# Optimization experiments

Measured on AMD Instinct MI355X. Metric: run time of the kernel, lower is better.

## Reference

```python
import jax, jax.numpy as jnp
import numpy as np

D_MODEL = 1024
NHEAD = 16
DK = D_MODEL // NHEAD  # 64
B, S = 2, 2048


def setup_inputs() -> dict:
    key = jax.random.key(0)
    ks = jax.random.split(key, 8)
    Q = jax.random.normal(ks[0], (B, S, D_MODEL), dtype=jnp.float32)
    K = jax.random.normal(ks[1], (B, S, D_MODEL), dtype=jnp.float32)
    V = jax.random.normal(ks[2], (B, S, D_MODEL), dtype=jnp.float32)
    additive_mask = jax.random.normal(ks[3], (S, S), dtype=jnp.float32)
    key_padding_mask = jnp.zeros((B, S), dtype=jnp.int32)  # ignored by the module
    # Per-head projection weights, stacked over heads: [H, d_model, dk]
    scale = 1.0 / np.sqrt(D_MODEL)
    WQ = jax.random.normal(ks[4], (NHEAD, D_MODEL, DK), dtype=jnp.float32) * scale
    WK = jax.random.normal(ks[5], (NHEAD, D_MODEL, DK), dtype=jnp.float32) * scale
    WV = jax.random.normal(ks[6], (NHEAD, D_MODEL, DK), dtype=jnp.float32) * scale
    WO = jax.random.normal(ks[7], (D_MODEL, D_MODEL), dtype=jnp.float32) * scale
    return {"Q": Q, "K": K, "V": V, "additive_mask": additive_mask,
            "key_padding_mask": key_padding_mask,
            "WQ": WQ, "WK": WK, "WV": WV, "WO": WO}


def reference(Q, K, V, additive_mask, key_padding_mask, WQ, WK, WV, WO):
    # Per-head projections, batched over heads: [B, H, S, dk]
    q = jnp.einsum('bsd,hdk->bhsk', Q, WQ)
    k = jnp.einsum('bsd,hdk->bhsk', K, WK)
    v = jnp.einsum('bsd,hdk->bhsk', V, WV)
    # scores: [B, H, S, S]; mask broadcasts over batch and head
    scores = jnp.einsum('bhqk,bhsk->bhqs', q, k) / np.sqrt(DK)
    scores = scores + additive_mask[None, None, :, :]
    attn = jax.nn.softmax(scores, axis=-1)
    o = jnp.einsum('bhqs,bhsk->bhqk', attn, v)  # [B, H, S, dk]
    # concat heads in head order == transpose + reshape to [B, S, H*dk]
    o = o.transpose(0, 2, 1, 3).reshape(Q.shape[0], Q.shape[1], D_MODEL)
    return o @ WO
```

## Files before the change

kernel.cpp:

```cpp
#include <hip/hip_runtime.h>
#include <hip/hip_bf16.h>
#include <stdint.h>

#define D_MODEL 1024
#define NHEAD 16
#define DKH 64
#define BATCH 2
#define SEQ 2048
#define LOG2E 1.44269504088896f

typedef __bf16 bf16_t;
typedef __bf16 bf16x8 __attribute__((ext_vector_type(8)));
typedef float f32x4 __attribute__((ext_vector_type(4)));

__device__ __forceinline__ float fast_exp2(float x) {
#if __has_builtin(__builtin_amdgcn_exp2f)
  return __builtin_amdgcn_exp2f(x);
#else
  return exp2f(x);
#endif
}

__device__ __forceinline__ void gload_lds16(const bf16_t* g, bf16_t* l) {
  auto gp = (const __attribute__((address_space(1))) void*)(uintptr_t)g;
  auto lp = (__attribute__((address_space(3))) void*)(uintptr_t)l;
  __builtin_amdgcn_global_load_lds(gp, lp, 16, 0, 0);
}

__global__ void k_cvt3(const float* __restrict__ Q, const float* __restrict__ K,
                       const float* __restrict__ V, bf16_t* __restrict__ out) {
  const float* in = blockIdx.y == 0 ? Q : (blockIdx.y == 1 ? K : V);
  int i = (blockIdx.x * 256 + threadIdx.x) * 8;
  float4 a = *reinterpret_cast<const float4*>(in + i);
  float4 b = *reinterpret_cast<const float4*>(in + i + 4);
  bf16x8 o;
  o[0] = (bf16_t)a.x; o[1] = (bf16_t)a.y; o[2] = (bf16_t)a.z; o[3] = (bf16_t)a.w;
  o[4] = (bf16_t)b.x; o[5] = (bf16_t)b.y; o[6] = (bf16_t)b.z; o[7] = (bf16_t)b.w;
  *reinterpret_cast<bf16x8*>(out + (size_t)blockIdx.y * BATCH * SEQ * D_MODEL + i) = o;
}

__global__ void k_cvtw(const float* __restrict__ WQ, const float* __restrict__ WK,
                       const float* __restrict__ WV, const float* __restrict__ WO,
                       bf16_t* __restrict__ wt) {
  int j = blockIdx.x * 256 + threadIdx.x;
  int d = j & 1023, n = j >> 10;
  if (n < 3072) {
    int proj = n >> 10, h = (n >> 6) & 15, k = n & 63;
    const float* w = proj == 0 ? WQ : (proj == 1 ? WK : WV);
    float scale = proj == 0 ? (0.125f * LOG2E) : 1.0f;
    wt[j] = (bf16_t)(w[(h << 16) + (d << 6) + k] * scale);
  } else {
    wt[j] = (bf16_t)WO[(d << 10) + (n - 3072)];
  }
}

__global__ void k_maskg(const float* __restrict__ M, bf16_t* __restrict__ Mf) {
  int t = blockIdx.x * 256 + threadIdx.x;
  int c = t & 3, lane = (t >> 2) & 63;
  int kvt = (t >> 8) & 31, qt16 = t >> 13;
  int q = qt16 * 16 + (lane & 15);
  int kv = kvt * 64 + c * 16 + ((lane >> 4) << 2);
  float4 m4 = *reinterpret_cast<const float4*>(M + (size_t)q * SEQ + kv);
  bf16_t o[4];
  o[0] = (bf16_t)(m4.x * LOG2E); o[1] = (bf16_t)(m4.y * LOG2E);
  o[2] = (bf16_t)(m4.z * LOG2E); o[3] = (bf16_t)(m4.w * LOG2E);
  *reinterpret_cast<ushort4*>(Mf + (size_t)t * 4) = *reinterpret_cast<ushort4*>(o);
}

__device__ __forceinline__ int vperm(int u) {
  return ((u >> 5) << 5) | (((u >> 2) & 3) << 3) | (((u >> 4) & 1) << 2) | (u & 3);
}

__global__ __launch_bounds__(256)
void k_gemm_qkv(const bf16_t* __restrict__ A, const bf16_t* __restrict__ Bt,
                bf16_t* __restrict__ qh, bf16_t* __restrict__ kh,
                bf16_t* __restrict__ vT) {
  __shared__ __align__(16) bf16_t As[128 * 32];
  __shared__ __align__(16) bf16_t Bs[128 * 32];
  const int tid = threadIdx.x;
  const int lane = tid & 63, wave = tid >> 6;
  const int g = lane >> 4, lr = lane & 15;
  const int bm = blockIdx.x, bn = blockIdx.y;
  const int pn = bn >> 3;
  const bf16_t* Ap = A + (size_t)pn * (BATCH * SEQ * D_MODEL);
  const int wm = (wave >> 1) << 6, wn = (wave & 1) << 6;
  f32x4 acc[4][4] = {};

  for (int kt = 0; kt < 1024; kt += 32) {
#pragma unroll
    for (int cc = 0; cc < 2; cc++) {
      int c = tid + cc * 256;
      int row = c >> 2, ko = (c & 3) << 3;
      gload_lds16(Ap + (size_t)(bm * 128 + row) * 1024 + kt + ko, As + c * 8);
      gload_lds16(Bt + (size_t)(bn * 128 + row) * 1024 + kt + ko, Bs + c * 8);
    }
    __syncthreads();
    bf16x8 af[4], bfr[4];
#pragma unroll
    for (int t = 0; t < 4; t++)
      af[t] = *reinterpret_cast<const bf16x8*>(As + (wm + t * 16 + lr) * 32 + g * 8);
#pragma unroll
    for (int t = 0; t < 4; t++)
      bfr[t] = *reinterpret_cast<const bf16x8*>(Bs + (wn + t * 16 + lr) * 32 + g * 8);
    __builtin_amdgcn_s_setprio(1);
#pragma unroll
    for (int i = 0; i < 4; i++)
#pragma unroll
      for (int j = 0; j < 4; j++)
        acc[i][j] = __builtin_amdgcn_mfma_f32_16x16x32_bf16(af[i], bfr[j], acc[i][j], 0, 0, 0);
    __builtin_amdgcn_s_setprio(0);
    __syncthreads();
  }

#pragma unroll
  for (int i = 0; i < 4; i++)
#pragma unroll
    for (int j = 0; j < 4; j++)
#pragma unroll
      for (int e = 0; e < 4; e++) {
        int row = (bm << 7) + wm + i * 16 + g * 4 + e;
        int col = ((bn & 7) << 7) + wn + j * 16 + lr;
        float v = acc[i][j][e];
        int b = row >> 11, s = row & 2047, h = col >> 6, kk = col & 63;
        if (pn == 0) {
          qh[((size_t)(((b << 4) + h) * SEQ + s) << 6) + kk] = (bf16_t)v;
        } else if (pn == 1) {
          kh[((size_t)(((b << 4) + h) * SEQ + s) << 6) + kk] = (bf16_t)v;
        } else {
          int s0 = s & ~63, u = s & 63;
          vT[((size_t)((((b << 4) + h) << 6) + kk) << 11) + s0 + vperm(u)] = (bf16_t)v;
        }
      }
}

__global__ __launch_bounds__(256)
void k_gemm_wo(const bf16_t* __restrict__ A, const bf16_t* __restrict__ Bt,
               float* __restrict__ C) {
  __shared__ __align__(16) bf16_t As[64 * 32];
  __shared__ __align__(16) bf16_t Bs[128 * 32];
  const int tid = threadIdx.x;
  const int lane = tid & 63, wave = tid >> 6;
  const int g = lane >> 4, lr = lane & 15;
  const int bm = blockIdx.x, bn = blockIdx.y;
  const int wm = (wave >> 1) << 5, wn = (wave & 1) << 6;
  f32x4 acc[2][4] = {};

  for (int kt = 0; kt < 1024; kt += 32) {
    {
      int row = tid >> 2, ko = (tid & 3) << 3;
      gload_lds16(A + (size_t)(bm * 64 + row) * 1024 + kt + ko, As + tid * 8);
    }
#pragma unroll
    for (int cc = 0; cc < 2; cc++) {
      int c = tid + cc * 256;
      int row = c >> 2, ko = (c & 3) << 3;
      gload_lds16(Bt + (size_t)(bn * 128 + row) * 1024 + kt + ko, Bs + c * 8);
    }
    __syncthreads();
    bf16x8 af[2], bfr[4];
#pragma unroll
    for (int t = 0; t < 2; t++)
      af[t] = *reinterpret_cast<const bf16x8*>(As + (wm + t * 16 + lr) * 32 + g * 8);
#pragma unroll
    for (int t = 0; t < 4; t++)
      bfr[t] = *reinterpret_cast<const bf16x8*>(Bs + (wn + t * 16 + lr) * 32 + g * 8);
    __builtin_amdgcn_s_setprio(1);
#pragma unroll
    for (int i = 0; i < 2; i++)
#pragma unroll
      for (int j = 0; j < 4; j++)
        acc[i][j] = __builtin_amdgcn_mfma_f32_16x16x32_bf16(af[i], bfr[j], acc[i][j], 0, 0, 0);
    __builtin_amdgcn_s_setprio(0);
    __syncthreads();
  }
#pragma unroll
  for (int i = 0; i < 2; i++)
#pragma unroll
    for (int j = 0; j < 4; j++)
#pragma unroll
      for (int e = 0; e < 4; e++) {
        int row = (bm << 6) + wm + i * 16 + g * 4 + e;
        int col = (bn << 7) + wn + j * 16 + lr;
        C[(size_t)row * D_MODEL + col] = acc[i][j][e];
      }
}

__global__ __launch_bounds__(512)
void k_attn4(const bf16_t* __restrict__ Qh, const bf16_t* __restrict__ Kh,
             const bf16_t* __restrict__ VTp, const bf16_t* __restrict__ Mf,
             bf16_t* __restrict__ O) {
  __shared__ __align__(16) bf16_t Ks[2][64 * 64];
  __shared__ __align__(16) bf16_t Vs[2][64 * 64];
  const int bh = blockIdx.y, b = bh >> 4, h = bh & 15;
  const int tid = threadIdx.x, wave = tid >> 6, lane = tid & 63;
  const int g = lane >> 4, lr = lane & 15;
  const int qbase = blockIdx.x * 128 + wave * 16;
  const bf16_t* qp = Qh + (size_t)bh * SEQ * DKH;
  const bf16_t* kp = Kh + (size_t)bh * SEQ * DKH;
  const bf16_t* vp = VTp + (size_t)bh * DKH * SEQ;
  const int qt16 = blockIdx.x * 8 + wave;
  const bf16_t* mp = Mf + ((size_t)qt16 * 32 * 64 + lane) * 16;

  bf16x8 aq[2];
#pragma unroll
  for (int ks = 0; ks < 2; ks++)
    aq[ks] = *reinterpret_cast<const bf16x8*>(
        qp + (size_t)(qbase + lr) * DKH + ks * 32 + g * 8);

  f32x4 oacc[4] = {};
  f32x4 lacc = {};
  const bf16_t onev = (bf16_t)1.0f;
  const bf16x8 ones = {onev, onev, onev, onev, onev, onev, onev, onev};

  auto stage = [&](int buf, int kv0) {
    int r = tid >> 3, u = tid & 7;
    int us = (u ^ (r & 7)) << 3;
    gload_lds16(kp + (size_t)(kv0 + r) * DKH + us, &Ks[buf][tid * 8]);
    gload_lds16(vp + (size_t)r * SEQ + kv0 + us, &Vs[buf][tid * 8]);
  };

  stage(0, 0);
  bf16x8 mva = *reinterpret_cast<const bf16x8*>(mp);
  bf16x8 mvb = *reinterpret_cast<const bf16x8*>(mp + 8);
  __syncthreads();

  for (int it = 0; it < SEQ / 64; ++it) {
    const int cur = it & 1;
    if (it + 1 < SEQ / 64) stage(cur ^ 1, (it + 1) * 64);
    bf16x8 mna = mva, mnb = mvb;
    if (it + 1 < SEQ / 64) {
      const bf16_t* mn = mp + (size_t)(it + 1) * 1024;
      mna = *reinterpret_cast<const bf16x8*>(mn);
      mnb = *reinterpret_cast<const bf16x8*>(mn + 8);
    }

    const bf16_t* kb = Ks[cur];
    const bf16_t* vb = Vs[cur];

    f32x4 p[4];
#pragma unroll
    for (int c = 0; c < 4; c++) {
      int r = c * 16 + lr;
      bf16x8 bk0 = *reinterpret_cast<const bf16x8*>(kb + r * 64 + ((g ^ (lr & 7)) << 3));
      bf16x8 bk1 = *reinterpret_cast<const bf16x8*>(kb + r * 64 + (((4 + g) ^ (lr & 7)) << 3));
      __builtin_amdgcn_s_setprio(1);
      f32x4 a = {};
      a = __builtin_amdgcn_mfma_f32_16x16x32_bf16(bk0, aq[0], a, 0, 0, 0);
      a = __builtin_amdgcn_mfma_f32_16x16x32_bf16(bk1, aq[1], a, 0, 0, 0);
      __builtin_amdgcn_s_setprio(0);
      p[c] = a;
    }

    bf16x8 pa[2];
#pragma unroll
    for (int c = 0; c < 4; c++)
#pragma unroll
      for (int e = 0; e < 4; e++) {
        int idx = c * 4 + e;
        float mk = (float)(idx < 8 ? mva[idx] : mvb[idx - 8]);
        float x = p[c][e] + mk;
        float pe = fast_exp2(fminf(x, 60.f));
        pa[c >> 1][(c & 1) * 4 + e] = (bf16_t)pe;
      }

    lacc = __builtin_amdgcn_mfma_f32_16x16x32_bf16(pa[0], ones, lacc, 0, 0, 0);
    lacc = __builtin_amdgcn_mfma_f32_16x16x32_bf16(pa[1], ones, lacc, 0, 0, 0);

#pragma unroll
    for (int c2 = 0; c2 < 4; c2++) {
      int r = c2 * 16 + lr;
      bf16x8 bv0 = *reinterpret_cast<const bf16x8*>(vb + r * 64 + ((g ^ (lr & 7)) << 3));
      bf16x8 bv1 = *reinterpret_cast<const bf16x8*>(vb + r * 64 + (((4 + g) ^ (lr & 7)) << 3));
      __builtin_amdgcn_s_setprio(1);
      oacc[c2] = __builtin_amdgcn_mfma_f32_16x16x32_bf16(pa[0], bv0, oacc[c2], 0, 0, 0);
      oacc[c2] = __builtin_amdgcn_mfma_f32_16x16x32_bf16(pa[1], bv1, oacc[c2], 0, 0, 0);
      __builtin_amdgcn_s_setprio(0);
    }
    __syncthreads();
    mva = mna; mvb = mnb;
  }

  float inv[4];
#pragma unroll
  for (int e = 0; e < 4; e++) inv[e] = 1.0f / lacc[e];
#pragma unroll
  for (int c2 = 0; c2 < 4; c2++)
#pragma unroll
    for (int e = 0; e < 4; e++) {
      float v = oacc[c2][e] * inv[e];
      int row = qbase + g * 4 + e;
      int col = (h << 6) + c2 * 16 + lr;
      O[(size_t)(b * SEQ + row) * D_MODEL + col] = (bf16_t)v;
    }
}

extern "C" void kernel_launch(void* const* d_in, const int* in_sizes, int n_in,
                              void* d_out, int out_size, void* d_ws, size_t ws_size,
                              hipStream_t stream) {
  const float* Q  = (const float*)d_in[0];
  const float* K  = (const float*)d_in[1];
  const float* V  = (const float*)d_in[2];
  const float* M  = (const float*)d_in[3];
  const float* WQ = (const float*)d_in[5];
  const float* WK = (const float*)d_in[6];
  const float* WV = (const float*)d_in[7];
  const float* WO = (const float*)d_in[8];

  char* ws = (char*)d_ws;
  const size_t MB = 1 << 20;
  bf16_t* Qb    = (bf16_t*)(ws + 0 * MB);
  bf16_t* Mf    = (bf16_t*)(ws + 24 * MB);
  bf16_t* WqkvT = (bf16_t*)(ws + 32 * MB);
  bf16_t* WoT   = (bf16_t*)(ws + 38 * MB);
  bf16_t* qh    = (bf16_t*)(ws + 40 * MB);
  bf16_t* kh    = (bf16_t*)(ws + 48 * MB);
  bf16_t* vT    = (bf16_t*)(ws + 56 * MB);
  bf16_t* Ob    = (bf16_t*)(ws + 64 * MB);

  k_cvt3<<<dim3(2048, 3), 256, 0, stream>>>(Q, K, V, Qb);
  k_maskg<<<4096, 256, 0, stream>>>(M, Mf);
  k_cvtw<<<16384, 256, 0, stream>>>(WQ, WK, WV, WO, WqkvT);

  k_gemm_qkv<<<dim3(32, 24), 256, 0, stream>>>(Qb, WqkvT, qh, kh, vT);

  k_attn4<<<dim3(16, 32), 512, 0, stream>>>(qh, kh, vT, Mf, Ob);

  k_gemm_wo<<<dim3(64, 8), 256, 0, stream>>>(Ob, WoT, (float*)d_out);
}
```

Measured before the change: 152.2 us.

## Rewrite attention with 32x32 MFMA tiles and split-KV across wave halves

Replaces the 16x16x32 MFMA attention kernel with one using 32x32x16 MFMAs. Each group of four waves processes half of the KV sequence, and the two partial outputs and row sums are combined through shared memory at the end. P fragments are repacked with v_permlane32_swap instead of relying on a pre-permuted V layout, so the V transpose write and the mask pre-layout are simplified. The row sum is now a scalar accumulation rather than an MFMA against a ones vector. This aims to cut instruction count and improve MFMA efficiency, at the cost of doubled LDS, a shared-memory reduction step, and a launch bound of 4 blocks per SIMD that may pressure registers.

```diff
diff --git a/kernel.cpp b/kernel.cpp
--- a/kernel.cpp
+++ b/kernel.cpp
@@ -12,6 +12,7 @@
 typedef __bf16 bf16_t;
 typedef __bf16 bf16x8 __attribute__((ext_vector_type(8)));
 typedef float f32x4 __attribute__((ext_vector_type(4)));
+typedef float f32x16 __attribute__((ext_vector_type(16)));
 
 __device__ __forceinline__ float fast_exp2(float x) {
 #if __has_builtin(__builtin_amdgcn_exp2f)
@@ -25,6 +26,18 @@
   auto gp = (const __attribute__((address_space(1))) void*)(uintptr_t)g;
   auto lp = (__attribute__((address_space(3))) void*)(uintptr_t)l;
   __builtin_amdgcn_global_load_lds(gp, lp, 16, 0, 0);
+}
+
+__device__ __forceinline__ uint32_t pkbf(float lo, float hi) {
+  bf16_t a = (bf16_t)lo, c = (bf16_t)hi;
+  uint16_t ua, uc;
+  __builtin_memcpy(&ua, &a, 2);
+  __builtin_memcpy(&uc, &c, 2);
+  return (uint32_t)ua | ((uint32_t)uc << 16);
+}
+
+__device__ __forceinline__ void perm32swap(uint32_t& a, uint32_t& b) {
+  asm volatile("v_permlane32_swap_b32 %0, %1" : "+v"(a), "+v"(b));
 }
 
 __global__ void k_cvt3(const float* __restrict__ Q, const float* __restrict__ K,
@@ -56,19 +69,17 @@
 
 __global__ void k_maskg(const float* __restrict__ M, bf16_t* __restrict__ Mf) {
   int t = blockIdx.x * 256 + threadIdx.x;
-  int c = t & 3, lane = (t >> 2) & 63;
-  int kvt = (t >> 8) & 31, qt16 = t >> 13;
-  int q = qt16 * 16 + (lane & 15);
-  int kv = kvt * 64 + c * 16 + ((lane >> 4) << 2);
-  float4 m4 = *reinterpret_cast<const float4*>(M + (size_t)q * SEQ + kv);
+  int wch = t & 7, lane = (t >> 3) & 63;
+  int kvt = (t >> 9) & 31, qt = t >> 14;
+  int h = lane >> 5, ql = lane & 31;
+  int q = qt * 32 + ql;
+  int t32 = wch >> 2, r2 = wch & 3;
+  int kvb = kvt * 64 + t32 * 32 + 8 * r2 + 4 * h;
+  float4 m4 = *reinterpret_cast<const float4*>(M + (size_t)q * SEQ + kvb);
   bf16_t o[4];
   o[0] = (bf16_t)(m4.x * LOG2E); o[1] = (bf16_t)(m4.y * LOG2E);
   o[2] = (bf16_t)(m4.z * LOG2E); o[3] = (bf16_t)(m4.w * LOG2E);
   *reinterpret_cast<ushort4*>(Mf + (size_t)t * 4) = *reinterpret_cast<ushort4*>(o);
-}
-
-__device__ __forceinline__ int vperm(int u) {
-  return ((u >> 5) << 5) | (((u >> 2) & 3) << 3) | (((u >> 4) & 1) << 2) | (u & 3);
 }
 
 __global__ __launch_bounds__(256)
@@ -127,8 +138,7 @@
         } else if (pn == 1) {
           kh[((size_t)(((b << 4) + h) * SEQ + s) << 6) + kk] = (bf16_t)v;
         } else {
-          int s0 = s & ~63, u = s & 63;
-          vT[((size_t)((((b << 4) + h) << 6) + kk) << 11) + s0 + vperm(u)] = (bf16_t)v;
+          vT[((size_t)((((b << 4) + h) << 6) + kk) << 11) + s] = (bf16_t)v;
         }
       }
 }
@@ -185,113 +195,163 @@
       }
 }
 
-__global__ __launch_bounds__(512)
-void k_attn4(const bf16_t* __restrict__ Qh, const bf16_t* __restrict__ Kh,
-             const bf16_t* __restrict__ VTp, const bf16_t* __restrict__ Mf,
+__global__ __launch_bounds__(512, 4)
+void k_attn5(const bf16_t* __restrict__ Qh, const bf16_t* __restrict__ Kh,
+             const bf16_t* __restrict__ VT, const bf16_t* __restrict__ Mf,
              bf16_t* __restrict__ O) {
-  __shared__ __align__(16) bf16_t Ks[2][64 * 64];
-  __shared__ __align__(16) bf16_t Vs[2][64 * 64];
+  __shared__ __align__(16) bf16_t Ks[2][2][4096];
+  __shared__ __align__(16) bf16_t Vs[2][2][4096];
   const int bh = blockIdx.y, b = bh >> 4, h = bh & 15;
-  const int tid = threadIdx.x, wave = tid >> 6, lane = tid & 63;
-  const int g = lane >> 4, lr = lane & 15;
-  const int qbase = blockIdx.x * 128 + wave * 16;
+  const int tid = threadIdx.x, w = tid >> 6, lane = tid & 63;
+  const int qw = w & 3, hh = w >> 2;
+  const int hq = lane >> 5, ql = lane & 31;
+  const int tid256 = tid & 255;
+  const int qbase = blockIdx.x * 128 + qw * 32;
   const bf16_t* qp = Qh + (size_t)bh * SEQ * DKH;
   const bf16_t* kp = Kh + (size_t)bh * SEQ * DKH;
-  const bf16_t* vp = VTp + (size_t)bh * DKH * SEQ;
-  const int qt16 = blockIdx.x * 8 + wave;
-  const bf16_t* mp = Mf + ((size_t)qt16 * 32 * 64 + lane) * 16;
-
-  bf16x8 aq[2];
-#pragma unroll
-  for (int ks = 0; ks < 2; ks++)
-    aq[ks] = *reinterpret_cast<const bf16x8*>(
-        qp + (size_t)(qbase + lr) * DKH + ks * 32 + g * 8);
-
-  f32x4 oacc[4] = {};
-  f32x4 lacc = {};
-  const bf16_t onev = (bf16_t)1.0f;
-  const bf16x8 ones = {onev, onev, onev, onev, onev, onev, onev, onev};
+  const bf16_t* vp = VT + (size_t)bh * DKH * SEQ;
+  const int qt = blockIdx.x * 4 + qw;
+  const bf16_t* mp = Mf + ((size_t)(qt * 32 + hh * 16) * 64 + lane) * 32;
+  const int NIT = 16;
+
+  bf16x8 aq[4];
+#pragma unroll
+  for (int kk = 0; kk < 4; kk++)
+    aq[kk] = *reinterpret_cast<const bf16x8*>(
+        qp + (size_t)(qbase + ql) * DKH + kk * 16 + hq * 8);
+
+  f32x16 oacc[2] = {};
+  float lsum = 0.f;
 
   auto stage = [&](int buf, int kv0) {
-    int r = tid >> 3, u = tid & 7;
-    int us = (u ^ (r & 7)) << 3;
-    gload_lds16(kp + (size_t)(kv0 + r) * DKH + us, &Ks[buf][tid * 8]);
-    gload_lds16(vp + (size_t)r * SEQ + kv0 + us, &Vs[buf][tid * 8]);
+#pragma unroll
+    for (int cc = 0; cc < 2; cc++) {
+      int c = tid256 + cc * 256;
+      int r = c >> 3, u = c & 7;
+      int us = (u ^ (r & 7)) << 3;
+      gload_lds16(kp + (size_t)(kv0 + r) * DKH + us, &Ks[hh][buf][c * 8]);
+      gload_lds16(vp + (size_t)r * SEQ + kv0 + us, &Vs[hh][buf][c * 8]);
+    }
   };
 
-  stage(0, 0);
-  bf16x8 mva = *reinterpret_cast<const bf16x8*>(mp);
-  bf16x8 mvb = *reinterpret_cast<const bf16x8*>(mp + 8);
+  stage(0, hh * 1024);
+  bf16x8 mv[4];
+#pragma unroll
+  for (int j = 0; j < 4; j++)
+    mv[j] = *reinterpret_cast<const bf16x8*>(mp + j * 8);
   __syncthreads();
 
-  for (int it = 0; it < SEQ / 64; ++it) {
+  for (int it = 0; it < NIT; ++it) {
     const int cur = it & 1;
-    if (it + 1 < SEQ / 64) stage(cur ^ 1, (it + 1) * 64);
-    bf16x8 mna = mva, mnb = mvb;
-    if (it + 1 < SEQ / 64) {
-      const bf16_t* mn = mp + (size_t)(it + 1) * 1024;
-      mna = *reinterpret_cast<const bf16x8*>(mn);
-      mnb = *reinterpret_cast<const bf16x8*>(mn + 8);
-    }
-
-    const bf16_t* kb = Ks[cur];
-    const bf16_t* vb = Vs[cur];
-
-    f32x4 p[4];
-#pragma unroll
-    for (int c = 0; c < 4; c++) {
-      int r = c * 16 + lr;
-      bf16x8 bk0 = *reinterpret_cast<const bf16x8*>(kb + r * 64 + ((g ^ (lr & 7)) << 3));
-      bf16x8 bk1 = *reinterpret_cast<const bf16x8*>(kb + r * 64 + (((4 + g) ^ (lr & 7)) << 3));
+    if (it + 1 < NIT) stage(cur ^ 1, hh * 1024 + (it + 1) * 64);
+
+    const bf16_t* kb = Ks[hh][cur];
+    const bf16_t* vb = Vs[hh][cur];
+
+    f32x16 p[2];
+#pragma unroll
+    for (int t32 = 0; t32 < 2; t32++) {
+      f32x16 a = {};
+      int r = t32 * 32 + ql;
       __builtin_amdgcn_s_setprio(1);
-      f32x4 a = {};
-      a = __builtin_amdgcn_mfma_f32_16x16x32_bf16(bk0, aq[0], a, 0, 0, 0);
-      a = __builtin_amdgcn_mfma_f32_16x16x32_bf16(bk1, aq[1], a, 0, 0, 0);
+#pragma unroll
+      for (int kk = 0; kk < 4; kk++) {
+        int us = ((kk * 2 + hq) ^ (r & 7)) << 3;
+        bf16x8 bk = *reinterpret_cast<const bf16x8*>(kb + r * 64 + us);
+        a = __builtin_amdgcn_mfma_f32_32x32x16_bf16(bk, aq[kk], a, 0, 0, 0);
+      }
       __builtin_amdgcn_s_setprio(0);
-      p[c] = a;
-    }
-
-    bf16x8 pa[2];
-#pragma unroll
-    for (int c = 0; c < 4; c++)
-#pragma unroll
-      for (int e = 0; e < 4; e++) {
-        int idx = c * 4 + e;
-        float mk = (float)(idx < 8 ? mva[idx] : mvb[idx - 8]);
-        float x = p[c][e] + mk;
+      p[t32] = a;
+    }
+
+    bf16x8 paf[4];
+#pragma unroll
+    for (int s = 0; s < 4; s++) {
+      const int t32 = s >> 1, rb = (s & 1) * 8;
+      float pes[8];
+#pragma unroll
+      for (int j = 0; j < 8; j++) {
+        int v = t32 * 16 + rb + j;
+        float x = p[t32][rb + j] + (float)mv[v >> 3][v & 7];
         float pe = fast_exp2(fminf(x, 60.f));
-        pa[c >> 1][(c & 1) * 4 + e] = (bf16_t)pe;
-      }
-
-    lacc = __builtin_amdgcn_mfma_f32_16x16x32_bf16(pa[0], ones, lacc, 0, 0, 0);
-    lacc = __builtin_amdgcn_mfma_f32_16x16x32_bf16(pa[1], ones, lacc, 0, 0, 0);
-
-#pragma unroll
-    for (int c2 = 0; c2 < 4; c2++) {
-      int r = c2 * 16 + lr;
-      bf16x8 bv0 = *reinterpret_cast<const bf16x8*>(vb + r * 64 + ((g ^ (lr & 7)) << 3));
-      bf16x8 bv1 = *reinterpret_cast<const bf16x8*>(vb + r * 64 + (((4 + g) ^ (lr & 7)) << 3));
+        lsum += pe;
+        pes[j] = pe;
+      }
+      uint32_t u0 = pkbf(pes[0], pes[1]), u1 = pkbf(pes[2], pes[3]);
+      uint32_t w0 = pkbf(pes[4], pes[5]), w1 = pkbf(pes[6], pes[7]);
+      perm32swap(u0, w0);
+      perm32swap(u1, w1);
+      union { uint32_t wd[4]; bf16x8 v8; } fu;
+      fu.wd[0] = u0; fu.wd[1] = u1; fu.wd[2] = w0; fu.wd[3] = w1;
+      paf[s] = fu.v8;
+    }
+
+    {
+      const bf16_t* mn = mp + (size_t)((it + 1 < NIT) ? (it + 1) : it) * 2048;
+#pragma unroll
+      for (int j = 0; j < 4; j++)
+        mv[j] = *reinterpret_cast<const bf16x8*>(mn + j * 8);
+    }
+
+#pragma unroll
+    for (int dkt = 0; dkt < 2; dkt++) {
+      int r = dkt * 32 + ql;
       __builtin_amdgcn_s_setprio(1);
-      oacc[c2] = __builtin_amdgcn_mfma_f32_16x16x32_bf16(pa[0], bv0, oacc[c2], 0, 0, 0);
-      oacc[c2] = __builtin_amdgcn_mfma_f32_16x16x32_bf16(pa[1], bv1, oacc[c2], 0, 0, 0);
+#pragma unroll
+      for (int s = 0; s < 4; s++) {
+        int us = ((2 * s + hq) ^ (r & 7)) << 3;
+        bf16x8 bv = *reinterpret_cast<const bf16x8*>(vb + r * 64 + us);
+        oacc[dkt] = __builtin_amdgcn_mfma_f32_32x32x16_bf16(paf[s], bv, oacc[dkt], 0, 0, 0);
+      }
       __builtin_amdgcn_s_setprio(0);
     }
     __syncthreads();
-    mva = mna; mvb = mnb;
-  }
-
-  float inv[4];
-#pragma unroll
-  for (int e = 0; e < 4; e++) inv[e] = 1.0f / lacc[e];
-#pragma unroll
-  for (int c2 = 0; c2 < 4; c2++)
-#pragma unroll
-    for (int e = 0; e < 4; e++) {
-      float v = oacc[c2][e] * inv[e];
-      int row = qbase + g * 4 + e;
-      int col = (h << 6) + c2 * 16 + lr;
-      O[(size_t)(b * SEQ + row) * D_MODEL + col] = (bf16_t)v;
-    }
+  }
+
+  float* smO = (float*)&Ks[0][0][0];
+  float* smL = (float*)&Vs[0][0][0];
+  if (w >= 4) {
+    int base = (qw * 64 + lane) * 32;
+#pragma unroll
+    for (int dkt = 0; dkt < 2; dkt++)
+#pragma unroll
+      for (int cg = 0; cg < 4; cg++) {
+        int chs = ((dkt * 4 + cg) ^ (lane & 7)) * 4;
+        float4 val = {oacc[dkt][cg * 4], oacc[dkt][cg * 4 + 1],
+                      oacc[dkt][cg * 4 + 2], oacc[dkt][cg * 4 + 3]};
+        *reinterpret_cast<float4*>(&smO[base + chs]) = val;
+      }
+    smL[qw * 64 + lane] = lsum;
+  }
+  __syncthreads();
+  if (w < 4) {
+    int base = (qw * 64 + lane) * 32;
+#pragma unroll
+    for (int dkt = 0; dkt < 2; dkt++)
+#pragma unroll
+      for (int cg = 0; cg < 4; cg++) {
+        int chs = ((dkt * 4 + cg) ^ (lane & 7)) * 4;
+        float4 pv = *reinterpret_cast<const float4*>(&smO[base + chs]);
+#pragma unroll
+        for (int e = 0; e < 4; e++) oacc[dkt][cg * 4 + e] += pv[e];
+      }
+    lsum += smL[qw * 64 + lane];
+    float lf = lsum + __shfl_xor(lsum, 32);
+    float inv[16];
+#pragma unroll
+    for (int reg = 0; reg < 16; reg++) {
+      int qrow = (reg & 3) + 8 * (reg >> 2) + 4 * hq;
+      inv[reg] = 1.0f / __shfl(lf, qrow);
+    }
+#pragma unroll
+    for (int dkt = 0; dkt < 2; dkt++)
+#pragma unroll
+      for (int reg = 0; reg < 16; reg++) {
+        int qrow = (reg & 3) + 8 * (reg >> 2) + 4 * hq;
+        float v = oacc[dkt][reg] * inv[reg];
+        O[(size_t)(b * SEQ + qbase + qrow) * D_MODEL + (h << 6) + dkt * 32 + ql] = (bf16_t)v;
+      }
+  }
 }
 
 extern "C" void kernel_launch(void* const* d_in, const int* in_sizes, int n_in,
@@ -323,7 +383,7 @@
 
   k_gemm_qkv<<<dim3(32, 24), 256, 0, stream>>>(Qb, WqkvT, qh, kh, vT);
 
-  k_attn4<<<dim3(16, 32), 512, 0, stream>>>(qh, kh, vT, Mf, Ob);
+  k_attn5<<<dim3(16, 32), 512, 0, stream>>>(qh, kh, vT, Mf, Ob);
 
   k_gemm_wo<<<dim3(64, 8), 256, 0, stream>>>(Ob, WoT, (float*)d_out);
 }
```

Result: slower. 161.8 us (+6.3%).

## Fuse fp32-to-bf16 activation conversion into QKV GEMM and remap blocks per XCD

Applied to the files above, without the earlier changes.

Drops the separate conversion kernel for Q/K/V. The QKV GEMM now reads fp32 activations directly, converts them in registers and writes bf16 into LDS, with the next tile's loads prefetched into registers. It also switches all three main kernels to 1D grids whose block index is remapped so that blocks sharing operands run on the same XCD, aiming for better L2 reuse. The trade-offs are twice the global read bytes for A inside the GEMM, and register-staged A loads instead of direct global-to-LDS loads.

```diff
diff --git a/kernel.cpp b/kernel.cpp
--- a/kernel.cpp
+++ b/kernel.cpp
@@ -25,18 +25,6 @@
   auto gp = (const __attribute__((address_space(1))) void*)(uintptr_t)g;
   auto lp = (__attribute__((address_space(3))) void*)(uintptr_t)l;
   __builtin_amdgcn_global_load_lds(gp, lp, 16, 0, 0);
-}
-
-__global__ void k_cvt3(const float* __restrict__ Q, const float* __restrict__ K,
-                       const float* __restrict__ V, bf16_t* __restrict__ out) {
-  const float* in = blockIdx.y == 0 ? Q : (blockIdx.y == 1 ? K : V);
-  int i = (blockIdx.x * 256 + threadIdx.x) * 8;
-  float4 a = *reinterpret_cast<const float4*>(in + i);
-  float4 b = *reinterpret_cast<const float4*>(in + i + 4);
-  bf16x8 o;
-  o[0] = (bf16_t)a.x; o[1] = (bf16_t)a.y; o[2] = (bf16_t)a.z; o[3] = (bf16_t)a.w;
-  o[4] = (bf16_t)b.x; o[5] = (bf16_t)b.y; o[6] = (bf16_t)b.z; o[7] = (bf16_t)b.w;
-  *reinterpret_cast<bf16x8*>(out + (size_t)blockIdx.y * BATCH * SEQ * D_MODEL + i) = o;
 }
 
 __global__ void k_cvtw(const float* __restrict__ WQ, const float* __restrict__ WK,
@@ -72,7 +60,8 @@
 }
 
 __global__ __launch_bounds__(256)
-void k_gemm_qkv(const bf16_t* __restrict__ A, const bf16_t* __restrict__ Bt,
+void k_gemm_qkv(const float* __restrict__ Qs, const float* __restrict__ Ks32,
+                const float* __restrict__ Vs32, const bf16_t* __restrict__ Bt,
                 bf16_t* __restrict__ qh, bf16_t* __restrict__ kh,
                 bf16_t* __restrict__ vT) {
   __shared__ __align__(16) bf16_t As[128 * 32];
@@ -80,19 +69,44 @@
   const int tid = threadIdx.x;
   const int lane = tid & 63, wave = tid >> 6;
   const int g = lane >> 4, lr = lane & 15;
-  const int bm = blockIdx.x, bn = blockIdx.y;
+  const int bid = blockIdx.x;
+  const int xcd = bid & 7, jj = bid >> 3;
+  const int bm = xcd * 4 + (jj & 3);
+  const int bn = jj >> 2;
   const int pn = bn >> 3;
-  const bf16_t* Ap = A + (size_t)pn * (BATCH * SEQ * D_MODEL);
+  const float* Ap32 = pn == 0 ? Qs : (pn == 1 ? Ks32 : Vs32);
   const int wm = (wave >> 1) << 6, wn = (wave & 1) << 6;
+  const int arow = tid >> 1, ako = (tid & 1) << 4;
+  const float* aptr = Ap32 + (size_t)(bm * 128 + arow) * 1024 + ako;
   f32x4 acc[4][4] = {};
+
+  float4 fA0 = *reinterpret_cast<const float4*>(aptr);
+  float4 fA1 = *reinterpret_cast<const float4*>(aptr + 4);
+  float4 fA2 = *reinterpret_cast<const float4*>(aptr + 8);
+  float4 fA3 = *reinterpret_cast<const float4*>(aptr + 12);
 
   for (int kt = 0; kt < 1024; kt += 32) {
 #pragma unroll
     for (int cc = 0; cc < 2; cc++) {
       int c = tid + cc * 256;
       int row = c >> 2, ko = (c & 3) << 3;
-      gload_lds16(Ap + (size_t)(bm * 128 + row) * 1024 + kt + ko, As + c * 8);
       gload_lds16(Bt + (size_t)(bn * 128 + row) * 1024 + kt + ko, Bs + c * 8);
+    }
+    {
+      bf16x8 o0, o1;
+      o0[0] = (bf16_t)fA0.x; o0[1] = (bf16_t)fA0.y; o0[2] = (bf16_t)fA0.z; o0[3] = (bf16_t)fA0.w;
+      o0[4] = (bf16_t)fA1.x; o0[5] = (bf16_t)fA1.y; o0[6] = (bf16_t)fA1.z; o0[7] = (bf16_t)fA1.w;
+      o1[0] = (bf16_t)fA2.x; o1[1] = (bf16_t)fA2.y; o1[2] = (bf16_t)fA2.z; o1[3] = (bf16_t)fA2.w;
+      o1[4] = (bf16_t)fA3.x; o1[5] = (bf16_t)fA3.y; o1[6] = (bf16_t)fA3.z; o1[7] = (bf16_t)fA3.w;
+      *reinterpret_cast<bf16x8*>(As + arow * 32 + ako) = o0;
+      *reinterpret_cast<bf16x8*>(As + arow * 32 + ako + 8) = o1;
+    }
+    if (kt + 32 < 1024) {
+      const float* np = aptr + kt + 32;
+      fA0 = *reinterpret_cast<const float4*>(np);
+      fA1 = *reinterpret_cast<const float4*>(np + 4);
+      fA2 = *reinterpret_cast<const float4*>(np + 8);
+      fA3 = *reinterpret_cast<const float4*>(np + 12);
     }
     __syncthreads();
     bf16x8 af[4], bfr[4];
@@ -121,14 +135,14 @@
         int row = (bm << 7) + wm + i * 16 + g * 4 + e;
         int col = ((bn & 7) << 7) + wn + j * 16 + lr;
         float v = acc[i][j][e];
-        int b = row >> 11, s = row & 2047, h = col >> 6, kk = col & 63;
+        int b = row >> 11, s = row & 2047, h = col >> 6, d = col & 63;
         if (pn == 0) {
-          qh[((size_t)(((b << 4) + h) * SEQ + s) << 6) + kk] = (bf16_t)v;
+          qh[((size_t)(((b << 4) + h) * SEQ + s) << 6) + d] = (bf16_t)v;
         } else if (pn == 1) {
-          kh[((size_t)(((b << 4) + h) * SEQ + s) << 6) + kk] = (bf16_t)v;
+          kh[((size_t)(((b << 4) + h) * SEQ + s) << 6) + d] = (bf16_t)v;
         } else {
           int s0 = s & ~63, u = s & 63;
-          vT[((size_t)((((b << 4) + h) << 6) + kk) << 11) + s0 + vperm(u)] = (bf16_t)v;
+          vT[((size_t)((((b << 4) + h) << 6) + d) << 11) + s0 + vperm(u)] = (bf16_t)v;
         }
       }
 }
@@ -141,7 +155,10 @@
   const int tid = threadIdx.x;
   const int lane = tid & 63, wave = tid >> 6;
   const int g = lane >> 4, lr = lane & 15;
-  const int bm = blockIdx.x, bn = blockIdx.y;
+  const int bid = blockIdx.x;
+  const int xcd = bid & 7, jj = bid >> 3;
+  const int bm = xcd * 8 + (jj & 7);
+  const int bn = jj >> 3;
   const int wm = (wave >> 1) << 5, wn = (wave & 1) << 6;
   f32x4 acc[2][4] = {};
 
@@ -191,14 +208,18 @@
              bf16_t* __restrict__ O) {
   __shared__ __align__(16) bf16_t Ks[2][64 * 64];
   __shared__ __align__(16) bf16_t Vs[2][64 * 64];
-  const int bh = blockIdx.y, b = bh >> 4, h = bh & 15;
+  const int bid = blockIdx.x;
+  const int xcd = bid & 7, loc = bid >> 3;
+  const int bh = xcd * 4 + (loc >> 4);
+  const int qtile = loc & 15;
+  const int b = bh >> 4, h = bh & 15;
   const int tid = threadIdx.x, wave = tid >> 6, lane = tid & 63;
   const int g = lane >> 4, lr = lane & 15;
-  const int qbase = blockIdx.x * 128 + wave * 16;
+  const int qbase = qtile * 128 + wave * 16;
   const bf16_t* qp = Qh + (size_t)bh * SEQ * DKH;
   const bf16_t* kp = Kh + (size_t)bh * SEQ * DKH;
   const bf16_t* vp = VTp + (size_t)bh * DKH * SEQ;
-  const int qt16 = blockIdx.x * 8 + wave;
+  const int qt16 = qtile * 8 + wave;
   const bf16_t* mp = Mf + ((size_t)qt16 * 32 * 64 + lane) * 16;
 
   bf16x8 aq[2];
@@ -308,7 +329,6 @@
 
   char* ws = (char*)d_ws;
   const size_t MB = 1 << 20;
-  bf16_t* Qb    = (bf16_t*)(ws + 0 * MB);
   bf16_t* Mf    = (bf16_t*)(ws + 24 * MB);
   bf16_t* WqkvT = (bf16_t*)(ws + 32 * MB);
   bf16_t* WoT   = (bf16_t*)(ws + 38 * MB);
@@ -317,13 +337,12 @@
   bf16_t* vT    = (bf16_t*)(ws + 56 * MB);
   bf16_t* Ob    = (bf16_t*)(ws + 64 * MB);
 
-  k_cvt3<<<dim3(2048, 3), 256, 0, stream>>>(Q, K, V, Qb);
   k_maskg<<<4096, 256, 0, stream>>>(M, Mf);
   k_cvtw<<<16384, 256, 0, stream>>>(WQ, WK, WV, WO, WqkvT);
 
-  k_gemm_qkv<<<dim3(32, 24), 256, 0, stream>>>(Qb, WqkvT, qh, kh, vT);
-
-  k_attn4<<<dim3(16, 32), 512, 0, stream>>>(qh, kh, vT, Mf, Ob);
-
-  k_gemm_wo<<<dim3(64, 8), 256, 0, stream>>>(Ob, WoT, (float*)d_out);
-}
+  k_gemm_qkv<<<768, 256, 0, stream>>>(Q, K, V, WqkvT, qh, kh, vT);
+
+  k_attn4<<<512, 512, 0, stream>>>(qh, kh, vT, Mf, Ob);
+
+  k_gemm_wo<<<512, 256, 0, stream>>>(Ob, WoT, (float*)d_out);
+}
```

After: 153.6 us. About the same (+0.9%).
